# Kernel optimization log

Hardware: AMD Instinct MI355X
Metric: run time of the kernel (lower is better)

## Reference

```python
import jax, jax.numpy as jnp
import numpy as np

B, S, D = 4, 4096, 1024

def setup_inputs() -> dict:
    key = jax.random.key(0)
    kx, kq, kk, kv = jax.random.split(key, 4)
    x = jax.random.normal(kx, (B, S, D), dtype=jnp.float32)
    # nn.Linear weights, stored here as [d_in, d_out] so y = x @ W
    scale = 1.0 / np.sqrt(D)
    Wq = jax.random.normal(kq, (D, D), dtype=jnp.float32) * scale
    Wk = jax.random.normal(kk, (D, D), dtype=jnp.float32) * scale
    Wv = jax.random.normal(kv, (D, D), dtype=jnp.float32) * scale
    return {"x": x, "Wq": Wq, "Wk": Wk, "Wv": Wv}

def reference(x, Wq, Wk, Wv):
    b, n, d_in = x.shape
    d_out = Wk.shape[1]
    q = jnp.einsum('bnd,de->bne', x, Wq)
    k = jnp.einsum('bnd,de,->bne', x, Wk, 1.0)  # keys
    v = jnp.einsum('bnd,de->bne', x, Wv)
    # full causal attention: scores scaled by 1/sqrt(d_out) AFTER masking (matches source)
    scores = jnp.einsum('bqe,bke->bqk', q, k)
    causal = jnp.triu(jnp.ones((n, n), dtype=bool), k=1)  # True above diagonal -> masked
    scores = jnp.where(causal[None, :, :], -jnp.inf, scores)
    attn = jax.nn.softmax(scores / jnp.sqrt(jnp.asarray(d_out, scores.dtype)), axis=-1)
    # dropout p=0.0 (eval) -> identity
    return jnp.einsum('bqk,bke->bqe', attn, v)
```

## Files before the change

### kernel.cpp

```cpp
#include <hip/hip_runtime.h>
#include <hip/hip_bf16.h>

#define B_ 4
#define S_ 4096
#define D_ 1024
#define NT_ 32
#define PAIRS_ 528

typedef __attribute__((ext_vector_type(8))) short short8;
typedef __attribute__((ext_vector_type(4))) float f32x4;

__device__ __forceinline__ unsigned short f2bf(float f) {
    union { float f; unsigned u; } v; v.f = f;
    unsigned u = v.u;
    return (unsigned short)((u + 0x7fffu + ((u >> 16) & 1u)) >> 16);
}

__device__ __forceinline__ void gld_lds16(const unsigned short* g, unsigned short* l) {
    __builtin_amdgcn_global_load_lds((const __attribute__((address_space(1))) void*)g,
                                     (__attribute__((address_space(3))) void*)l, 16, 0, 0);
}

__device__ __forceinline__ void stage128x32(const unsigned short* gbase, size_t ld,
                                            unsigned short* ls, int tid) {
    const int r = tid >> 2;
    const int c = (tid & 3) * 8;
    unsigned short* lw = ls + tid * 8;
    gld_lds16(gbase + (size_t)r * ld + c, lw);
    gld_lds16(gbase + (size_t)(r + 64) * ld + c, lw + 2048);
}

__global__ __launch_bounds__(256) void prep_x(const float* __restrict__ x,
                                              unsigned short* __restrict__ xb) {
    size_t i = ((size_t)blockIdx.x * 256 + threadIdx.x) * 8;
    float4 a = *(const float4*)&x[i];
    float4 b = *(const float4*)&x[i + 4];
    unsigned u0 = (unsigned)f2bf(a.x) | ((unsigned)f2bf(a.y) << 16);
    unsigned u1 = (unsigned)f2bf(a.z) | ((unsigned)f2bf(a.w) << 16);
    unsigned u2 = (unsigned)f2bf(b.x) | ((unsigned)f2bf(b.y) << 16);
    unsigned u3 = (unsigned)f2bf(b.z) | ((unsigned)f2bf(b.w) << 16);
    uint4 val; val.x = u0; val.y = u1; val.z = u2; val.w = u3;
    *(uint4*)&xb[i] = val;
}

__global__ __launch_bounds__(256) void prep_w(const float* __restrict__ Wq,
                                              const float* __restrict__ Wk,
                                              const float* __restrict__ Wv,
                                              unsigned short* __restrict__ Wt) {
    __shared__ float ls[64 * 65];
    const int z = blockIdx.z;
    const float* __restrict__ W = (z == 0) ? Wq : (z == 1) ? Wk : Wv;
    unsigned short* __restrict__ Wtz = Wt + (size_t)z * D_ * D_;
    const int k0 = blockIdx.y * 64, n0 = blockIdx.x * 64;
    const int tid = threadIdx.x;
    #pragma unroll
    for (int i = 0; i < 16; ++i) {
        int lin = i * 256 + tid, r = lin >> 6, c = lin & 63;
        ls[r * 65 + c] = W[(size_t)(k0 + r) * D_ + n0 + c];
    }
    __syncthreads();
    #pragma unroll
    for (int i = 0; i < 16; ++i) {
        int lin = i * 256 + tid, r = lin >> 6, c = lin & 63;
        Wtz[(size_t)(n0 + r) * D_ + k0 + c] = f2bf(ls[c * 65 + r]);
    }
}

__global__ __launch_bounds__(512, 2) void qkv_gemm(
    const unsigned short* __restrict__ xb, const unsigned short* __restrict__ Wt,
    unsigned short* __restrict__ Q, unsigned short* __restrict__ K,
    unsigned short* __restrict__ V)
{
    __shared__ __align__(16) unsigned short lsA[2 * 256 * 64];
    __shared__ __align__(16) unsigned short lsB[2 * 256 * 64];

    const int z = blockIdx.z;
    unsigned short* __restrict__ Y = (z == 0) ? Q : (z == 1) ? K : V;
    const float scale = (z == 0) ? 0.03125f : 1.0f;

    const int lin = blockIdx.x;
    const int wg = (lin & 7) * 32 + (lin >> 3);
    const int m0 = (wg >> 2) * 256, n0 = (wg & 3) * 256;

    const int tid = threadIdx.x, lane = tid & 63, w = tid >> 6;
    const int wm = w >> 2, wn = w & 3;
    const int quad = lane >> 4, ln = lane & 15;

    const unsigned short* Ab = xb + (size_t)m0 * D_;
    const unsigned short* Bb = Wt + (size_t)z * D_ * D_ + (size_t)n0 * D_;

#define STAGE_HALF(gbase, ldsbase)                                              \
    {                                                                           \
        _Pragma("unroll")                                                       \
        for (int i_ = 0; i_ < 2; ++i_) {                                        \
            int g_ = tid + i_ * 512;                                            \
            int r_ = g_ >> 3;                                                   \
            int cg_ = (g_ & 7) ^ (r_ & 7);                                      \
            gld_lds16((gbase) + (size_t)r_ * D_ + cg_ * 8, (ldsbase) + g_ * 8); \
        }                                                                       \
    }
#define STAGE(kt, h)                                                                   \
    {                                                                                  \
        if ((h) < 2) { STAGE_HALF(Ab + (size_t)((h) * 128) * D_ + (kt) * 64,           \
                                  &lsA[(((kt) & 1) * 2 + (h)) * 8192]) }               \
        else         { STAGE_HALF(Bb + (size_t)(((h) - 2) * 128) * D_ + (kt) * 64,     \
                                  &lsB[(((kt) & 1) * 2 + ((h) - 2)) * 8192]) }         \
    }

    const unsigned short* As;
    const unsigned short* Bs;
    short8 a[4][2], b[2][2];
    f32x4 acc[8][4] = {};

#define LDA(mh)                                                                        \
    {                                                                                  \
        _Pragma("unroll")                                                              \
        for (int mf_ = 0; mf_ < 4; ++mf_) {                                            \
            _Pragma("unroll")                                                          \
            for (int ks_ = 0; ks_ < 2; ++ks_) {                                        \
                int r_ = wm * 128 + ((mh) * 4 + mf_) * 16 + ln;                        \
                int cg_ = ks_ * 4 + quad;                                              \
                a[mf_][ks_] = *(const short8*)&As[r_ * 64 + ((cg_ ^ (r_ & 7)) << 3)];  \
            }                                                                          \
        }                                                                              \
    }
#define LDB(nh)                                                                        \
    {                                                                                  \
        _Pragma("unroll")                                                              \
        for (int nf_ = 0; nf_ < 2; ++nf_) {                                            \
            _Pragma("unroll")                                                          \
            for (int ks_ = 0; ks_ < 2; ++ks_) {                                        \
                int r_ = wn * 64 + ((nh) * 2 + nf_) * 16 + ln;                         \
                int cg_ = ks_ * 4 + quad;                                              \
                b[nf_][ks_] = *(const short8*)&Bs[r_ * 64 + ((cg_ ^ (r_ & 7)) << 3)];  \
            }                                                                          \
        }                                                                              \
    }
#define MM(mh, nh)                                                                     \
    {                                                                                  \
        __builtin_amdgcn_s_setprio(1);                                                 \
        _Pragma("unroll")                                                              \
        for (int mf_ = 0; mf_ < 4; ++mf_)                                              \
            _Pragma("unroll")                                                          \
            for (int nf_ = 0; nf_ < 2; ++nf_)                                          \
                _Pragma("unroll")                                                      \
                for (int ks_ = 0; ks_ < 2; ++ks_)                                      \
                    acc[(mh) * 4 + mf_][(nh) * 2 + nf_] =                              \
                        __builtin_amdgcn_mfma_f32_16x16x32_bf16(                       \
                            a[mf_][ks_], b[nf_][ks_],                                  \
                            acc[(mh) * 4 + mf_][(nh) * 2 + nf_], 0, 0, 0);             \
        __builtin_amdgcn_s_setprio(0);                                                 \
    }
#define LGKM0 asm volatile("s_waitcnt lgkmcnt(0)" ::: "memory")
#define VM0   asm volatile("s_waitcnt vmcnt(0)" ::: "memory")
#define BAR   __builtin_amdgcn_s_barrier()
#define SB0   __builtin_amdgcn_sched_barrier(0)

    STAGE(0, 0) STAGE(0, 1) STAGE(0, 2) STAGE(0, 3)
    VM0; SB0;
    BAR; SB0;

    #pragma unroll 2
    for (int t = 0; t < 16; ++t) {
        As = lsA + (t & 1) * 16384;
        Bs = lsB + (t & 1) * 16384;
        if (t < 15) { STAGE(t + 1, 0) STAGE(t + 1, 1) STAGE(t + 1, 2) STAGE(t + 1, 3) }
        SB0;
        LDA(0) LDB(0)
        MM(0, 0)
        LDB(1)
        MM(0, 1)
        LDA(1)
        MM(1, 1)
        LDB(0)
        MM(1, 0)
        LGKM0; SB0;
        if (t < 15) {
            VM0; SB0;
            BAR; SB0;
        }
    }

#undef STAGE_HALF
#undef STAGE
#undef LDA
#undef LDB
#undef MM
#undef LGKM0
#undef VM0
#undef BAR
#undef SB0

    #pragma unroll
    for (int mf = 0; mf < 8; ++mf)
        #pragma unroll
        for (int nf = 0; nf < 4; ++nf)
            #pragma unroll
            for (int rr = 0; rr < 4; ++rr) {
                int row = m0 + wm * 128 + mf * 16 + quad * 4 + rr;
                int col = n0 + wn * 64 + nf * 16 + ln;
                Y[(size_t)row * D_ + col] = f2bf(acc[mf][nf][rr] * scale);
            }
}

__global__ __launch_bounds__(256) void vt_trans(const unsigned short* __restrict__ V,
                                                unsigned short* __restrict__ Vt) {
    __shared__ unsigned short ls[64 * 66];
    const int s0 = blockIdx.x * 64, e0 = blockIdx.y * 64, b = blockIdx.z;
    const int tid = threadIdx.x;
    const size_t base = (size_t)b * S_ * D_;
    #pragma unroll
    for (int i = 0; i < 16; ++i) {
        int lin = i * 256 + tid, r = lin >> 6, c = lin & 63;
        ls[r * 66 + c] = V[base + (size_t)(s0 + r) * D_ + e0 + c];
    }
    __syncthreads();
    const size_t baseT = (size_t)b * D_ * S_;
    #pragma unroll
    for (int i = 0; i < 16; ++i) {
        int lin = i * 256 + tid, r = lin >> 6, c = lin & 63;
        Vt[baseT + (size_t)(e0 + r) * S_ + s0 + c] = ls[c * 66 + r];
    }
}

__global__ __launch_bounds__(256) void qk_pexp(
    const unsigned short* __restrict__ Q, const unsigned short* __restrict__ K,
    unsigned short* __restrict__ P, float* __restrict__ lpart)
{
    __shared__ __align__(16) unsigned short lsA[4096];
    __shared__ __align__(16) unsigned short lsB[4096];
    __shared__ float sml[2][128];

    const int l = blockIdx.x, b = blockIdx.y;
    const int r = l & 7;
    const int s = l >> 3;
    int qt, kt;
    if (s < r + 1)            { qt = r;      kt = s; }
    else if (s < 33)          { qt = 31 - r; kt = s - (r + 1); }
    else if (s < 42 + r)      { qt = 8 + r;  kt = s - 33; }
    else                      { qt = 23 - r; kt = s - (42 + r); }
    const int p = qt * (qt + 1) / 2 + kt;

    const int q0 = qt * 128, k0 = kt * 128;
    const int tid = threadIdx.x, lane = tid & 63, w = tid >> 6;
    const int wm = w >> 1, wn = w & 1, quad = lane >> 4, ln = lane & 15;
    const size_t base = (size_t)b * S_ * D_;

    const unsigned short* Qb = Q + base + (size_t)q0 * D_;
    const unsigned short* Kb = K + base + (size_t)k0 * D_;

    f32x4 acc[4][4] = {};
    for (int et = 0; et < D_ / 32; ++et) {
        stage128x32(Qb + et * 32, D_, lsA, tid);
        stage128x32(Kb + et * 32, D_, lsB, tid);
        __syncthreads();
        short8 af[4], bfr[4];
        #pragma unroll
        for (int mf = 0; mf < 4; ++mf)
            af[mf] = *(const short8*)&lsA[(wm * 64 + mf * 16 + ln) * 32 + quad * 8];
        #pragma unroll
        for (int nf = 0; nf < 4; ++nf)
            bfr[nf] = *(const short8*)&lsB[(wn * 64 + nf * 16 + ln) * 32 + quad * 8];
        #pragma unroll
        for (int mf = 0; mf < 4; ++mf)
            #pragma unroll
            for (int nf = 0; nf < 4; ++nf)
                acc[mf][nf] = __builtin_amdgcn_mfma_f32_16x16x32_bf16(af[mf], bfr[nf], acc[mf][nf], 0, 0, 0);
        __syncthreads();
    }

    const bool diag = (kt == qt);
    unsigned short* Pt = P + ((size_t)b * PAIRS_ + p) * (128 * 128);

    #pragma unroll
    for (int mf = 0; mf < 4; ++mf)
        #pragma unroll
        for (int rr = 0; rr < 4; ++rr) {
            int rowq = wm * 64 + mf * 16 + quad * 4 + rr;
            float lsum = 0.0f;
            #pragma unroll
            for (int nf = 0; nf < 4; ++nf) {
                int ckey = wn * 64 + nf * 16 + ln;
                float sc = acc[mf][nf][rr];
                float pe = (diag && ckey > rowq) ? 0.0f : __expf(fminf(sc, 60.0f));
                Pt[rowq * 128 + ckey] = f2bf(pe);
                lsum += pe;
            }
            #pragma unroll
            for (int off = 1; off < 16; off <<= 1)
                lsum += __shfl_xor(lsum, off);
            if (ln == 0) sml[wn][rowq] = lsum;
        }
    __syncthreads();

    if (tid < 128)
        lpart[((size_t)b * PAIRS_ + p) * 128 + tid] = sml[0][tid] + sml[1][tid];
}

__global__ __launch_bounds__(128) void merge_il(const float* __restrict__ lpart,
                                                float* __restrict__ il) {
    const int qt = blockIdx.x, b = blockIdx.y;
    const int row = threadIdx.x;
    const int pbase = qt * (qt + 1) / 2;
    float l = 0.0f;
    for (int kt = 0; kt <= qt; ++kt)
        l += lpart[((size_t)b * PAIRS_ + pbase + kt) * 128 + row];
    il[(size_t)b * S_ + qt * 128 + row] = 1.0f / l;
}

__global__ __launch_bounds__(256) void pv_gemm(
    const unsigned short* __restrict__ P, const unsigned short* __restrict__ Vt,
    const float* __restrict__ il, float* __restrict__ O)
{
    __shared__ __align__(16) unsigned short lsA[4096];
    __shared__ __align__(16) unsigned short lsB[4096];

    const int l = blockIdx.x;
    const int dt = l & 7;
    const int s = l >> 3;
    const int pair = s & 15;
    const int b = s >> 4;
    const int d0 = dt * 128;
    const int tid = threadIdx.x, lane = tid & 63, w = tid >> 6;
    const int wm = w >> 1, wn = w & 1, quad = lane >> 4, ln = lane & 15;

    const unsigned short* Vtb = Vt + ((size_t)b * D_ + d0) * S_;

    #pragma unroll 1
    for (int half = 0; half < 2; ++half) {
        const int qt = half ? pair : (31 - pair);
        const int q0 = qt * 128;
        const int pbase = qt * (qt + 1) / 2;

        f32x4 acc[4][4] = {};

        #pragma unroll 1
        for (int ktile = 0; ktile <= qt; ++ktile) {
            const unsigned short* Ptile = P + ((size_t)b * PAIRS_ + pbase + ktile) * (128 * 128);
            #pragma unroll 1
            for (int sub = 0; sub < 4; ++sub) {
                stage128x32(Ptile + sub * 32, 128, lsA, tid);
                stage128x32(Vtb + ktile * 128 + sub * 32, S_, lsB, tid);
                __syncthreads();
                short8 af[4], bfr[4];
                #pragma unroll
                for (int mf = 0; mf < 4; ++mf)
                    af[mf] = *(const short8*)&lsA[(wm * 64 + mf * 16 + ln) * 32 + quad * 8];
                #pragma unroll
                for (int nf = 0; nf < 4; ++nf)
                    bfr[nf] = *(const short8*)&lsB[(wn * 64 + nf * 16 + ln) * 32 + quad * 8];
                #pragma unroll
                for (int mf = 0; mf < 4; ++mf)
                    #pragma unroll
                    for (int nf = 0; nf < 4; ++nf)
                        acc[mf][nf] = __builtin_amdgcn_mfma_f32_16x16x32_bf16(af[mf], bfr[nf], acc[mf][nf], 0, 0, 0);
                __syncthreads();
            }
        }

        #pragma unroll
        for (int mf = 0; mf < 4; ++mf) {
            float ilv[4];
            #pragma unroll
            for (int rr = 0; rr < 4; ++rr)
                ilv[rr] = il[(size_t)b * S_ + q0 + wm * 64 + mf * 16 + quad * 4 + rr];
            #pragma unroll
            for (int nf = 0; nf < 4; ++nf)
                #pragma unroll
                for (int rr = 0; rr < 4; ++rr) {
                    int rowq = q0 + wm * 64 + mf * 16 + quad * 4 + rr;
                    int col = d0 + wn * 64 + nf * 16 + ln;
                    O[((size_t)b * S_ + rowq) * D_ + col] = acc[mf][nf][rr] * ilv[rr];
                }
        }
    }
}

extern "C" void kernel_launch(void* const* d_in, const int* in_sizes, int n_in,
                              void* d_out, int out_size, void* d_ws, size_t ws_size,
                              hipStream_t stream) {
    const float* x  = (const float*)d_in[0];
    const float* Wq = (const float*)d_in[1];
    const float* Wk = (const float*)d_in[2];
    const float* Wv = (const float*)d_in[3];

    const size_t nQ = (size_t)B_ * S_ * D_;
    const size_t nP = (size_t)B_ * PAIRS_ * 128 * 128;

    unsigned short* P  = (unsigned short*)d_ws;
    unsigned short* V  = P;
    unsigned short* Q  = P + nP;
    unsigned short* K  = Q + nQ;
    unsigned short* Vt = K + nQ;
    unsigned short* xb = Vt;
    unsigned short* Wt = Vt + nQ;
    float* lpart = (float*)(Wt + (size_t)3 * D_ * D_);
    float* il    = lpart + (size_t)B_ * PAIRS_ * 128;
    float* O = (float*)d_out;

    hipLaunchKernelGGL(prep_x, dim3(8192), dim3(256), 0, stream, x, xb);
    hipLaunchKernelGGL(prep_w, dim3(16, 16, 3), dim3(256), 0, stream, Wq, Wk, Wv, Wt);
    hipLaunchKernelGGL(qkv_gemm, dim3(256, 1, 3), dim3(512), 0, stream, xb, Wt, Q, K, V);
    hipLaunchKernelGGL(vt_trans, dim3(64, 16, B_), dim3(256), 0, stream, V, Vt);
    hipLaunchKernelGGL(qk_pexp, dim3(PAIRS_, B_), dim3(256), 0, stream, Q, K, P, lpart);
    hipLaunchKernelGGL(merge_il, dim3(NT_, B_), dim3(128), 0, stream, lpart, il);
    hipLaunchKernelGGL(pv_gemm, dim3(512), dim3(256), 0, stream, P, Vt, il, O);
}
```

Measured before the change: 442.1 us.

## Triple-buffer GEMM pipelines and fuse V transpose into QKV epilogue

Rewrites the QKV, QK and PV GEMM main loops to use a three-stage LDS ring fed by global_load_lds with swizzled 32-wide K slices, waiting on vmcnt(4) so two tiles stay in flight. The V projection now writes its transposed output directly through an LDS staging buffer, which removes the separate vt_trans kernel and one round trip of V through memory. The PV kernel also remaps its block index to group d-tiles, and the QK and PV kernels get occupancy hints. In exchange, LDS use rises, register pressure may rise, and the hand-placed waits and barriers are fragile.

```diff
diff --git a/kernel.cpp b/kernel.cpp
--- a/kernel.cpp
+++ b/kernel.cpp
@@ -21,14 +21,11 @@
                                      (__attribute__((address_space(3))) void*)l, 16, 0, 0);
 }
 
-__device__ __forceinline__ void stage128x32(const unsigned short* gbase, size_t ld,
-                                            unsigned short* ls, int tid) {
-    const int r = tid >> 2;
-    const int c = (tid & 3) * 8;
-    unsigned short* lw = ls + tid * 8;
-    gld_lds16(gbase + (size_t)r * ld + c, lw);
-    gld_lds16(gbase + (size_t)(r + 64) * ld + c, lw + 2048);
-}
+#define LGKM0 asm volatile("s_waitcnt lgkmcnt(0)" ::: "memory")
+#define VM0   asm volatile("s_waitcnt vmcnt(0)" ::: "memory")
+#define VM4   asm volatile("s_waitcnt vmcnt(4)" ::: "memory")
+#define BAR   __builtin_amdgcn_s_barrier()
+#define SB0   __builtin_amdgcn_sched_barrier(0)
 
 __global__ __launch_bounds__(256) void prep_x(const float* __restrict__ x,
                                               unsigned short* __restrict__ xb) {
@@ -69,13 +66,11 @@
 __global__ __launch_bounds__(512, 2) void qkv_gemm(
     const unsigned short* __restrict__ xb, const unsigned short* __restrict__ Wt,
     unsigned short* __restrict__ Q, unsigned short* __restrict__ K,
-    unsigned short* __restrict__ V)
+    unsigned short* __restrict__ Vt)
 {
-    __shared__ __align__(16) unsigned short lsA[2 * 256 * 64];
-    __shared__ __align__(16) unsigned short lsB[2 * 256 * 64];
+    __shared__ __align__(16) unsigned short ls[3 * 16384];
 
     const int z = blockIdx.z;
-    unsigned short* __restrict__ Y = (z == 0) ? Q : (z == 1) ? K : V;
     const float scale = (z == 0) ? 0.03125f : 1.0f;
 
     const int lin = blockIdx.x;
@@ -89,146 +84,126 @@
     const unsigned short* Ab = xb + (size_t)m0 * D_;
     const unsigned short* Bb = Wt + (size_t)z * D_ * D_ + (size_t)n0 * D_;
 
-#define STAGE_HALF(gbase, ldsbase)                                              \
-    {                                                                           \
-        _Pragma("unroll")                                                       \
-        for (int i_ = 0; i_ < 2; ++i_) {                                        \
-            int g_ = tid + i_ * 512;                                            \
-            int r_ = g_ >> 3;                                                   \
-            int cg_ = (g_ & 7) ^ (r_ & 7);                                      \
-            gld_lds16((gbase) + (size_t)r_ * D_ + cg_ * 8, (ldsbase) + g_ * 8); \
-        }                                                                       \
-    }
-#define STAGE(kt, h)                                                                   \
-    {                                                                                  \
-        if ((h) < 2) { STAGE_HALF(Ab + (size_t)((h) * 128) * D_ + (kt) * 64,           \
-                                  &lsA[(((kt) & 1) * 2 + (h)) * 8192]) }               \
-        else         { STAGE_HALF(Bb + (size_t)(((h) - 2) * 128) * D_ + (kt) * 64,     \
-                                  &lsB[(((kt) & 1) * 2 + ((h) - 2)) * 8192]) }         \
-    }
-
-    const unsigned short* As;
-    const unsigned short* Bs;
-    short8 a[4][2], b[2][2];
+#define QKV_STAGE(kt, r)                                                          \
+    {                                                                             \
+        _Pragma("unroll")                                                         \
+        for (int i_ = 0; i_ < 2; ++i_) {                                          \
+            int g_ = tid + i_ * 512;                                              \
+            int row_ = g_ >> 2;                                                   \
+            int gs_ = (g_ & 3) ^ ((row_ >> 1) & 3);                               \
+            gld_lds16(Ab + (size_t)row_ * D_ + (kt) * 32 + gs_ * 8,               \
+                      ls + (r) * 16384 + g_ * 8);                                 \
+            gld_lds16(Bb + (size_t)row_ * D_ + (kt) * 32 + gs_ * 8,               \
+                      ls + (r) * 16384 + 8192 + g_ * 8);                          \
+        }                                                                         \
+    }
+
     f32x4 acc[8][4] = {};
 
-#define LDA(mh)                                                                        \
-    {                                                                                  \
-        _Pragma("unroll")                                                              \
-        for (int mf_ = 0; mf_ < 4; ++mf_) {                                            \
-            _Pragma("unroll")                                                          \
-            for (int ks_ = 0; ks_ < 2; ++ks_) {                                        \
-                int r_ = wm * 128 + ((mh) * 4 + mf_) * 16 + ln;                        \
-                int cg_ = ks_ * 4 + quad;                                              \
-                a[mf_][ks_] = *(const short8*)&As[r_ * 64 + ((cg_ ^ (r_ & 7)) << 3)];  \
-            }                                                                          \
-        }                                                                              \
-    }
-#define LDB(nh)                                                                        \
-    {                                                                                  \
-        _Pragma("unroll")                                                              \
-        for (int nf_ = 0; nf_ < 2; ++nf_) {                                            \
-            _Pragma("unroll")                                                          \
-            for (int ks_ = 0; ks_ < 2; ++ks_) {                                        \
-                int r_ = wn * 64 + ((nh) * 2 + nf_) * 16 + ln;                         \
-                int cg_ = ks_ * 4 + quad;                                              \
-                b[nf_][ks_] = *(const short8*)&Bs[r_ * 64 + ((cg_ ^ (r_ & 7)) << 3)];  \
-            }                                                                          \
-        }                                                                              \
-    }
-#define MM(mh, nh)                                                                     \
-    {                                                                                  \
-        __builtin_amdgcn_s_setprio(1);                                                 \
-        _Pragma("unroll")                                                              \
-        for (int mf_ = 0; mf_ < 4; ++mf_)                                              \
-            _Pragma("unroll")                                                          \
-            for (int nf_ = 0; nf_ < 2; ++nf_)                                          \
-                _Pragma("unroll")                                                      \
-                for (int ks_ = 0; ks_ < 2; ++ks_)                                      \
-                    acc[(mh) * 4 + mf_][(nh) * 2 + nf_] =                              \
-                        __builtin_amdgcn_mfma_f32_16x16x32_bf16(                       \
-                            a[mf_][ks_], b[nf_][ks_],                                  \
-                            acc[(mh) * 4 + mf_][(nh) * 2 + nf_], 0, 0, 0);             \
-        __builtin_amdgcn_s_setprio(0);                                                 \
-    }
-#define LGKM0 asm volatile("s_waitcnt lgkmcnt(0)" ::: "memory")
-#define VM0   asm volatile("s_waitcnt vmcnt(0)" ::: "memory")
-#define BAR   __builtin_amdgcn_s_barrier()
-#define SB0   __builtin_amdgcn_sched_barrier(0)
-
-    STAGE(0, 0) STAGE(0, 1) STAGE(0, 2) STAGE(0, 3)
-    VM0; SB0;
+#define QKV_BODY(r)                                                              \
+    {                                                                            \
+        const unsigned short* As_ = ls + (r) * 16384;                            \
+        const unsigned short* Bs_ = As_ + 8192;                                  \
+        short8 a_[8], b_[4];                                                     \
+        _Pragma("unroll")                                                        \
+        for (int mf_ = 0; mf_ < 8; ++mf_) {                                      \
+            int row_ = wm * 128 + mf_ * 16 + ln;                                 \
+            int g_ = quad ^ ((row_ >> 1) & 3);                                   \
+            a_[mf_] = *(const short8*)&As_[row_ * 32 + g_ * 8];                  \
+        }                                                                        \
+        _Pragma("unroll")                                                        \
+        for (int nf_ = 0; nf_ < 4; ++nf_) {                                      \
+            int row_ = wn * 64 + nf_ * 16 + ln;                                  \
+            int g_ = quad ^ ((row_ >> 1) & 3);                                   \
+            b_[nf_] = *(const short8*)&Bs_[row_ * 32 + g_ * 8];                  \
+        }                                                                        \
+        __builtin_amdgcn_s_setprio(1);                                          \
+        _Pragma("unroll")                                                        \
+        for (int mf_ = 0; mf_ < 8; ++mf_)                                        \
+            _Pragma("unroll")                                                    \
+            for (int nf_ = 0; nf_ < 4; ++nf_)                                    \
+                acc[mf_][nf_] = __builtin_amdgcn_mfma_f32_16x16x32_bf16(         \
+                    a_[mf_], b_[nf_], acc[mf_][nf_], 0, 0, 0);                   \
+        __builtin_amdgcn_s_setprio(0);                                          \
+    }
+
+#define QKV_STEP(t, r, rn, wcode)                                                \
+    {                                                                            \
+        if ((wcode) == 0) QKV_STAGE((t) + 2, rn)                                 \
+        SB0;                                                                     \
+        QKV_BODY(r)                                                              \
+        LGKM0; SB0;                                                              \
+        if ((wcode) == 0)      { VM4; SB0; BAR; SB0; }                           \
+        else if ((wcode) == 1) { VM0; SB0; BAR; SB0; }                           \
+    }
+
+    QKV_STAGE(0, 0) QKV_STAGE(1, 1)
+    VM4; SB0;
     BAR; SB0;
 
-    #pragma unroll 2
-    for (int t = 0; t < 16; ++t) {
-        As = lsA + (t & 1) * 16384;
-        Bs = lsB + (t & 1) * 16384;
-        if (t < 15) { STAGE(t + 1, 0) STAGE(t + 1, 1) STAGE(t + 1, 2) STAGE(t + 1, 3) }
-        SB0;
-        LDA(0) LDB(0)
-        MM(0, 0)
-        LDB(1)
-        MM(0, 1)
-        LDA(1)
-        MM(1, 1)
-        LDB(0)
-        MM(1, 0)
-        LGKM0; SB0;
-        if (t < 15) {
-            VM0; SB0;
-            BAR; SB0;
+    #pragma unroll 1
+    for (int tb = 0; tb < 30; tb += 3) {
+        QKV_STEP(tb,     0, 2, 0)
+        QKV_STEP(tb + 1, 1, 0, 0)
+        QKV_STEP(tb + 2, 2, 1, 0)
+    }
+    QKV_STEP(30, 0, 0, 1)
+    QKV_STEP(31, 1, 0, 2)
+
+#undef QKV_STAGE
+#undef QKV_BODY
+#undef QKV_STEP
+
+    if (z != 2) {
+        unsigned short* __restrict__ Y = (z == 0) ? Q : K;
+        #pragma unroll
+        for (int mf = 0; mf < 8; ++mf)
+            #pragma unroll
+            for (int nf = 0; nf < 4; ++nf)
+                #pragma unroll
+                for (int rr = 0; rr < 4; ++rr) {
+                    int row = m0 + wm * 128 + mf * 16 + quad * 4 + rr;
+                    int col = n0 + wn * 64 + nf * 16 + ln;
+                    Y[(size_t)row * D_ + col] = f2bf(acc[mf][nf][rr] * scale);
+                }
+    } else {
+        BAR;
+        unsigned int* U = (unsigned int*)ls + w * 2080;
+        const int b_ = m0 >> 12;
+        const int sbase = (m0 & 4095) + wm * 128;
+        unsigned int* VtU = (unsigned int*)Vt;
+        #pragma unroll
+        for (int ch = 0; ch < 2; ++ch) {
+            #pragma unroll
+            for (int nfl = 0; nfl < 2; ++nfl) {
+                int nf = ch * 2 + nfl;
+                int el = nfl * 16 + ln;
+                #pragma unroll
+                for (int mf = 0; mf < 8; ++mf)
+                    #pragma unroll
+                    for (int pr = 0; pr < 2; ++pr) {
+                        unsigned lo = f2bf(acc[mf][nf][2 * pr]);
+                        unsigned hi = f2bf(acc[mf][nf][2 * pr + 1]);
+                        U[el * 65 + mf * 8 + quad * 2 + pr] = lo | (hi << 16);
+                    }
+            }
+            LGKM0; SB0;
+            #pragma unroll 4
+            for (int el = 0; el < 32; ++el) {
+                unsigned v = U[el * 65 + lane];
+                int eg = n0 + wn * 64 + ch * 32 + el;
+                VtU[(((size_t)b_ * D_ + eg) * S_ + sbase) / 2 + lane] = v;
+            }
+            if (ch == 0) { LGKM0; SB0; }
         }
     }
-
-#undef STAGE_HALF
-#undef STAGE
-#undef LDA
-#undef LDB
-#undef MM
-#undef LGKM0
-#undef VM0
-#undef BAR
-#undef SB0
-
-    #pragma unroll
-    for (int mf = 0; mf < 8; ++mf)
-        #pragma unroll
-        for (int nf = 0; nf < 4; ++nf)
-            #pragma unroll
-            for (int rr = 0; rr < 4; ++rr) {
-                int row = m0 + wm * 128 + mf * 16 + quad * 4 + rr;
-                int col = n0 + wn * 64 + nf * 16 + ln;
-                Y[(size_t)row * D_ + col] = f2bf(acc[mf][nf][rr] * scale);
-            }
-}
-
-__global__ __launch_bounds__(256) void vt_trans(const unsigned short* __restrict__ V,
-                                                unsigned short* __restrict__ Vt) {
-    __shared__ unsigned short ls[64 * 66];
-    const int s0 = blockIdx.x * 64, e0 = blockIdx.y * 64, b = blockIdx.z;
-    const int tid = threadIdx.x;
-    const size_t base = (size_t)b * S_ * D_;
-    #pragma unroll
-    for (int i = 0; i < 16; ++i) {
-        int lin = i * 256 + tid, r = lin >> 6, c = lin & 63;
-        ls[r * 66 + c] = V[base + (size_t)(s0 + r) * D_ + e0 + c];
-    }
-    __syncthreads();
-    const size_t baseT = (size_t)b * D_ * S_;
-    #pragma unroll
-    for (int i = 0; i < 16; ++i) {
-        int lin = i * 256 + tid, r = lin >> 6, c = lin & 63;
-        Vt[baseT + (size_t)(e0 + r) * S_ + s0 + c] = ls[c * 66 + r];
-    }
-}
-
-__global__ __launch_bounds__(256) void qk_pexp(
+}
+
+__global__ __launch_bounds__(256, 3) void qk_pexp(
     const unsigned short* __restrict__ Q, const unsigned short* __restrict__ K,
     unsigned short* __restrict__ P, float* __restrict__ lpart)
 {
-    __shared__ __align__(16) unsigned short lsA[4096];
-    __shared__ __align__(16) unsigned short lsB[4096];
+    __shared__ __align__(16) unsigned short ls[3 * 8192];
     __shared__ float sml[2][128];
 
     const int l = blockIdx.x, b = blockIdx.y;
@@ -249,25 +224,75 @@
     const unsigned short* Qb = Q + base + (size_t)q0 * D_;
     const unsigned short* Kb = K + base + (size_t)k0 * D_;
 
+#define QK_STAGE(kt_, r_)                                                         \
+    {                                                                             \
+        _Pragma("unroll")                                                         \
+        for (int i_ = 0; i_ < 2; ++i_) {                                          \
+            int g_ = tid + i_ * 256;                                              \
+            int row_ = g_ >> 2;                                                   \
+            int gs_ = (g_ & 3) ^ ((row_ >> 1) & 3);                               \
+            gld_lds16(Qb + (size_t)row_ * D_ + (kt_) * 32 + gs_ * 8,              \
+                      ls + (r_) * 8192 + g_ * 8);                                 \
+            gld_lds16(Kb + (size_t)row_ * D_ + (kt_) * 32 + gs_ * 8,              \
+                      ls + (r_) * 8192 + 4096 + g_ * 8);                          \
+        }                                                                         \
+    }
+
     f32x4 acc[4][4] = {};
-    for (int et = 0; et < D_ / 32; ++et) {
-        stage128x32(Qb + et * 32, D_, lsA, tid);
-        stage128x32(Kb + et * 32, D_, lsB, tid);
-        __syncthreads();
-        short8 af[4], bfr[4];
-        #pragma unroll
-        for (int mf = 0; mf < 4; ++mf)
-            af[mf] = *(const short8*)&lsA[(wm * 64 + mf * 16 + ln) * 32 + quad * 8];
-        #pragma unroll
-        for (int nf = 0; nf < 4; ++nf)
-            bfr[nf] = *(const short8*)&lsB[(wn * 64 + nf * 16 + ln) * 32 + quad * 8];
-        #pragma unroll
-        for (int mf = 0; mf < 4; ++mf)
-            #pragma unroll
-            for (int nf = 0; nf < 4; ++nf)
-                acc[mf][nf] = __builtin_amdgcn_mfma_f32_16x16x32_bf16(af[mf], bfr[nf], acc[mf][nf], 0, 0, 0);
-        __syncthreads();
-    }
+
+#define QK_BODY(r_)                                                              \
+    {                                                                            \
+        const unsigned short* As_ = ls + (r_) * 8192;                            \
+        const unsigned short* Bs_ = As_ + 4096;                                  \
+        short8 a_[4], b_[4];                                                     \
+        _Pragma("unroll")                                                        \
+        for (int mf_ = 0; mf_ < 4; ++mf_) {                                      \
+            int row_ = wm * 64 + mf_ * 16 + ln;                                  \
+            int g_ = quad ^ ((row_ >> 1) & 3);                                   \
+            a_[mf_] = *(const short8*)&As_[row_ * 32 + g_ * 8];                  \
+        }                                                                        \
+        _Pragma("unroll")                                                        \
+        for (int nf_ = 0; nf_ < 4; ++nf_) {                                      \
+            int row_ = wn * 64 + nf_ * 16 + ln;                                  \
+            int g_ = quad ^ ((row_ >> 1) & 3);                                   \
+            b_[nf_] = *(const short8*)&Bs_[row_ * 32 + g_ * 8];                  \
+        }                                                                        \
+        __builtin_amdgcn_s_setprio(1);                                          \
+        _Pragma("unroll")                                                        \
+        for (int mf_ = 0; mf_ < 4; ++mf_)                                        \
+            _Pragma("unroll")                                                    \
+            for (int nf_ = 0; nf_ < 4; ++nf_)                                    \
+                acc[mf_][nf_] = __builtin_amdgcn_mfma_f32_16x16x32_bf16(         \
+                    a_[mf_], b_[nf_], acc[mf_][nf_], 0, 0, 0);                   \
+        __builtin_amdgcn_s_setprio(0);                                          \
+    }
+
+#define QK_STEP(t, r_, rn, wcode)                                                \
+    {                                                                            \
+        if ((wcode) == 0) QK_STAGE((t) + 2, rn)                                  \
+        SB0;                                                                     \
+        QK_BODY(r_)                                                              \
+        LGKM0; SB0;                                                              \
+        if ((wcode) == 0)      { VM4; SB0; BAR; SB0; }                           \
+        else if ((wcode) == 1) { VM0; SB0; BAR; SB0; }                           \
+    }
+
+    QK_STAGE(0, 0) QK_STAGE(1, 1)
+    VM4; SB0;
+    BAR; SB0;
+
+    #pragma unroll 1
+    for (int tb = 0; tb < 30; tb += 3) {
+        QK_STEP(tb,     0, 2, 0)
+        QK_STEP(tb + 1, 1, 0, 0)
+        QK_STEP(tb + 2, 2, 1, 0)
+    }
+    QK_STEP(30, 0, 0, 1)
+    QK_STEP(31, 1, 0, 2)
+
+#undef QK_STAGE
+#undef QK_BODY
+#undef QK_STEP
 
     const bool diag = (kt == qt);
     unsigned short* Pt = P + ((size_t)b * PAIRS_ + p) * (128 * 128);
@@ -308,54 +333,90 @@
     il[(size_t)b * S_ + qt * 128 + row] = 1.0f / l;
 }
 
-__global__ __launch_bounds__(256) void pv_gemm(
+__global__ __launch_bounds__(256, 3) void pv_gemm(
     const unsigned short* __restrict__ P, const unsigned short* __restrict__ Vt,
     const float* __restrict__ il, float* __restrict__ O)
 {
-    __shared__ __align__(16) unsigned short lsA[4096];
-    __shared__ __align__(16) unsigned short lsB[4096];
-
-    const int l = blockIdx.x;
-    const int dt = l & 7;
-    const int s = l >> 3;
-    const int pair = s & 15;
-    const int b = s >> 4;
+    __shared__ __align__(16) unsigned short ls[3 * 8192];
+
+    const int bid = blockIdx.x;
+    const int u  = (bid & 7) | ((bid >> 6) << 3);
+    const int dt = (bid >> 3) & 7;
+    const int pair = u & 15;
+    const int b = u >> 4;
     const int d0 = dt * 128;
     const int tid = threadIdx.x, lane = tid & 63, w = tid >> 6;
     const int wm = w >> 1, wn = w & 1, quad = lane >> 4, ln = lane & 15;
 
     const unsigned short* Vtb = Vt + ((size_t)b * D_ + d0) * S_;
+
+#define PV_STAGE(c_, r_)                                                          \
+    {                                                                             \
+        const unsigned short* Pt_ = Pbase + (size_t)((c_) >> 2) * (128 * 128);    \
+        _Pragma("unroll")                                                         \
+        for (int i_ = 0; i_ < 2; ++i_) {                                          \
+            int g_ = tid + i_ * 256;                                              \
+            int row_ = g_ >> 2;                                                   \
+            int gs_ = (g_ & 3) ^ ((row_ >> 1) & 3);                               \
+            gld_lds16(Pt_ + (size_t)row_ * 128 + ((c_) & 3) * 32 + gs_ * 8,       \
+                      ls + (r_) * 8192 + g_ * 8);                                 \
+            gld_lds16(Vtb + (size_t)row_ * S_ + (c_) * 32 + gs_ * 8,              \
+                      ls + (r_) * 8192 + 4096 + g_ * 8);                          \
+        }                                                                         \
+    }
+
+#define PV_BODY(r_)                                                              \
+    {                                                                            \
+        const unsigned short* As_ = ls + (r_) * 8192;                            \
+        const unsigned short* Bs_ = As_ + 4096;                                  \
+        short8 a_[4], b_[4];                                                     \
+        _Pragma("unroll")                                                        \
+        for (int mf_ = 0; mf_ < 4; ++mf_) {                                      \
+            int row_ = wm * 64 + mf_ * 16 + ln;                                  \
+            int g_ = quad ^ ((row_ >> 1) & 3);                                   \
+            a_[mf_] = *(const short8*)&As_[row_ * 32 + g_ * 8];                  \
+        }                                                                        \
+        _Pragma("unroll")                                                        \
+        for (int nf_ = 0; nf_ < 4; ++nf_) {                                      \
+            int row_ = wn * 64 + nf_ * 16 + ln;                                  \
+            int g_ = quad ^ ((row_ >> 1) & 3);                                   \
+            b_[nf_] = *(const short8*)&Bs_[row_ * 32 + g_ * 8];                  \
+        }                                                                        \
+        __builtin_amdgcn_s_setprio(1);                                          \
+        _Pragma("unroll")                                                        \
+        for (int mf_ = 0; mf_ < 4; ++mf_)                                        \
+            _Pragma("unroll")                                                    \
+            for (int nf_ = 0; nf_ < 4; ++nf_)                                    \
+                acc[mf_][nf_] = __builtin_amdgcn_mfma_f32_16x16x32_bf16(         \
+                    a_[mf_], b_[nf_], acc[mf_][nf_], 0, 0, 0);                   \
+        __builtin_amdgcn_s_setprio(0);                                          \
+    }
 
     #pragma unroll 1
     for (int half = 0; half < 2; ++half) {
         const int qt = half ? pair : (31 - pair);
         const int q0 = qt * 128;
         const int pbase = qt * (qt + 1) / 2;
+        const int nst = 4 * (qt + 1);
+        const unsigned short* Pbase = P + ((size_t)b * PAIRS_ + pbase) * (128 * 128);
 
         f32x4 acc[4][4] = {};
 
+        if (half) { BAR; SB0; }
+        PV_STAGE(0, 0) PV_STAGE(1, 1)
+        VM4; SB0;
+        BAR; SB0;
+
         #pragma unroll 1
-        for (int ktile = 0; ktile <= qt; ++ktile) {
-            const unsigned short* Ptile = P + ((size_t)b * PAIRS_ + pbase + ktile) * (128 * 128);
-            #pragma unroll 1
-            for (int sub = 0; sub < 4; ++sub) {
-                stage128x32(Ptile + sub * 32, 128, lsA, tid);
-                stage128x32(Vtb + ktile * 128 + sub * 32, S_, lsB, tid);
-                __syncthreads();
-                short8 af[4], bfr[4];
-                #pragma unroll
-                for (int mf = 0; mf < 4; ++mf)
-                    af[mf] = *(const short8*)&lsA[(wm * 64 + mf * 16 + ln) * 32 + quad * 8];
-                #pragma unroll
-                for (int nf = 0; nf < 4; ++nf)
-                    bfr[nf] = *(const short8*)&lsB[(wn * 64 + nf * 16 + ln) * 32 + quad * 8];
-                #pragma unroll
-                for (int mf = 0; mf < 4; ++mf)
-                    #pragma unroll
-                    for (int nf = 0; nf < 4; ++nf)
-                        acc[mf][nf] = __builtin_amdgcn_mfma_f32_16x16x32_bf16(af[mf], bfr[nf], acc[mf][nf], 0, 0, 0);
-                __syncthreads();
-            }
+        for (int t = 0; t < nst; ++t) {
+            const int r_ = t % 3;
+            if (t + 2 < nst) { const int rn_ = (t + 2) % 3; PV_STAGE(t + 2, rn_) }
+            SB0;
+            PV_BODY(r_)
+            LGKM0; SB0;
+            if (t + 2 < nst)      { VM4; SB0; }
+            else if (t + 1 < nst) { VM0; SB0; }
+            if (t + 1 < nst) { BAR; SB0; }
         }
 
         #pragma unroll
@@ -374,6 +435,8 @@
                 }
         }
     }
+#undef PV_STAGE
+#undef PV_BODY
 }
 
 extern "C" void kernel_launch(void* const* d_in, const int* in_sizes, int n_in,
@@ -388,11 +451,10 @@
     const size_t nP = (size_t)B_ * PAIRS_ * 128 * 128;
 
     unsigned short* P  = (unsigned short*)d_ws;
-    unsigned short* V  = P;
+    unsigned short* xb = P;
     unsigned short* Q  = P + nP;
     unsigned short* K  = Q + nQ;
     unsigned short* Vt = K + nQ;
-    unsigned short* xb = Vt;
     unsigned short* Wt = Vt + nQ;
     float* lpart = (float*)(Wt + (size_t)3 * D_ * D_);
     float* il    = lpart + (size_t)B_ * PAIRS_ * 128;
@@ -400,8 +462,7 @@
 
     hipLaunchKernelGGL(prep_x, dim3(8192), dim3(256), 0, stream, x, xb);
     hipLaunchKernelGGL(prep_w, dim3(16, 16, 3), dim3(256), 0, stream, Wq, Wk, Wv, Wt);
-    hipLaunchKernelGGL(qkv_gemm, dim3(256, 1, 3), dim3(512), 0, stream, xb, Wt, Q, K, V);
-    hipLaunchKernelGGL(vt_trans, dim3(64, 16, B_), dim3(256), 0, stream, V, Vt);
+    hipLaunchKernelGGL(qkv_gemm, dim3(256, 1, 3), dim3(512), 0, stream, xb, Wt, Q, K, Vt);
     hipLaunchKernelGGL(qk_pexp, dim3(PAIRS_, B_), dim3(256), 0, stream, Q, K, P, lpart);
     hipLaunchKernelGGL(merge_il, dim3(NT_, B_), dim3(128), 0, stream, lpart, il);
     hipLaunchKernelGGL(pv_gemm, dim3(512), dim3(256), 0, stream, P, Vt, il, O);
```

After: 423.7 us. 1.04x faster.
